# Kernel tuning notes

Measured on AMD Instinct MI355X. Metric: run time of the kernel, lower is better.

Reference implementation:

```python
import jax, jax.numpy as jnp
import numpy as np

NUM_NODES = 50000

def _gat_conv(x, edge_index, W, a_src, a_dst, b):
    # PyG GATConv, heads=1: h = x W ; e_ij = LeakyReLU(a_src.h_j + a_dst.h_i)
    # softmax over incoming edges of i ; out_i = sum_j alpha_ij h_j + b
    h = x @ W                                  # [N, F]
    src, dst = edge_index[0], edge_index[1]    # edge j->i : src=j, dst=i
    alpha_s = h @ a_src                        # [N]
    alpha_d = h @ a_dst                        # [N]
    e = jax.nn.leaky_relu(alpha_s[src] + alpha_d[dst], negative_slope=0.2)  # [E]
    # segment softmax over destination nodes
    e_max = jax.ops.segment_max(e, dst, num_segments=NUM_NODES)
    e_exp = jnp.exp(e - e_max[dst])
    denom = jax.ops.segment_sum(e_exp, dst, num_segments=NUM_NODES)
    coef = e_exp / denom[dst]                  # [E]
    out = jax.ops.segment_sum(h[src] * coef[:, None], dst, num_segments=NUM_NODES)
    return out + b

def setup_inputs() -> dict:
    key = jax.random.key(0)
    ks = jax.random.split(key, 10)
    N, E, IN, HID, OUT = NUM_NODES, 800000, 256, 256, 128
    x = jax.random.normal(ks[0], (N, IN), dtype=jnp.float32)
    edge_index = jax.random.randint(ks[1], (2, E), 0, N, dtype=jnp.int32)
    def glorot(k, shape):
        lim = float(np.sqrt(6.0 / (shape[0] + shape[-1])))
        return jax.random.uniform(k, shape, jnp.float32, -lim, lim)
    return {
        'x': x,
        'edge_index': edge_index,
        'W1': glorot(ks[2], (IN, HID)),
        'a_src1': glorot(ks[3], (HID,)),
        'a_dst1': glorot(ks[4], (HID,)),
        'b1': jnp.zeros((HID,), jnp.float32),
        'W2': glorot(ks[5], (HID, OUT)),
        'a_src2': glorot(ks[6], (OUT,)),
        'a_dst2': glorot(ks[7], (OUT,)),
        'b2': jnp.zeros((OUT,), jnp.float32),
    }

def reference(x, edge_index, W1, a_src1, a_dst1, b1, W2, a_src2, a_dst2, b2):
    # add self loops once (same edge_index used by both convs)
    ar = jnp.arange(NUM_NODES, dtype=edge_index.dtype)
    ei = jnp.concatenate([edge_index, jnp.stack([ar, ar])], axis=1)
    x1 = _gat_conv(x, ei, W1, a_src1, a_dst1, b1)
    h = jax.nn.relu(x1)          # dropout p=0.3 is identity in eval mode
    x2 = _gat_conv(h, ei, W2, a_src2, a_dst2, b2)
    return (x2, h)
```

## Files before the change

kernel.cpp:

```cpp
#include <hip/hip_runtime.h>
#include <hip/hip_bf16.h>

#define N_NODES 50000
#define E0      800000
#define ETOT    850000

typedef __bf16 bf16x8 __attribute__((ext_vector_type(8)));
typedef float  f32x4  __attribute__((ext_vector_type(4)));
typedef ushort u16x8  __attribute__((ext_vector_type(8)));
union B8 { u16x8 u; bf16x8 b; };

static __device__ __forceinline__ float b2f(ushort u) {
    union { uint u; float f; } x; x.u = ((uint)u) << 16; return x.f;
}
static __device__ __forceinline__ ushort f2bf(float f) {
    uint u = __builtin_bit_cast(uint, f);
    uint r = (u + 0x7FFFu + ((u >> 16) & 1u)) >> 16;
    return (ushort)r;
}

static __device__ __forceinline__ void gload16(const ushort* g, ushort* l) {
    __builtin_amdgcn_global_load_lds((const __attribute__((address_space(1))) unsigned int*)g,
                                     (__attribute__((address_space(3))) unsigned int*)l, 16, 0, 0);
}


__global__ __launch_bounds__(256) void k_deg(const int* __restrict__ ei, int* __restrict__ deg) {
    int e = blockIdx.x * 256 + threadIdx.x;
    if (e >= ETOT) return;
    int dst = (e < E0) ? ei[E0 + e] : (e - E0);
    atomicAdd(&deg[dst], 1);
}

__global__ __launch_bounds__(256) void k_scan1(const int* __restrict__ deg, int* __restrict__ offs,
                                               int* __restrict__ bsum) {
    __shared__ int buf[256];
    int tid = threadIdx.x;
    int i = blockIdx.x * 256 + tid;
    int v = (i < N_NODES) ? deg[i] : 0;
    buf[tid] = v;
    __syncthreads();
    for (int off = 1; off < 256; off <<= 1) {
        int t = (tid >= off) ? buf[tid - off] : 0;
        __syncthreads();
        buf[tid] += t;
        __syncthreads();
    }
    if (i < N_NODES) offs[i + 1] = buf[tid];
    if (tid == 255) bsum[blockIdx.x] = buf[255];
}

__global__ __launch_bounds__(256) void k_scan2(int* __restrict__ bsum, int nb) {
    __shared__ int buf[256];
    int tid = threadIdx.x;
    int v = (tid < nb) ? bsum[tid] : 0;
    buf[tid] = v;
    __syncthreads();
    for (int off = 1; off < 256; off <<= 1) {
        int t = (tid >= off) ? buf[tid - off] : 0;
        __syncthreads();
        buf[tid] += t;
        __syncthreads();
    }
    if (tid < nb) bsum[tid] = buf[tid] - v;
}

__global__ __launch_bounds__(256) void k_scan3(int* __restrict__ offs, const int* __restrict__ bsum,
                                               int* __restrict__ cursor) {
    int tid = threadIdx.x;
    int i = blockIdx.x * 256 + tid;
    if (i < N_NODES) {
        int v = offs[i + 1] + bsum[blockIdx.x];
        offs[i + 1] = v;
        cursor[i + 1] = v;
    }
    if (i == 0) { offs[0] = 0; cursor[0] = 0; }
}

__global__ __launch_bounds__(256) void k_scatter(const int* __restrict__ ei, int* __restrict__ cursor,
                                                 int* __restrict__ esrc) {
    int e = blockIdx.x * 256 + threadIdx.x;
    if (e >= ETOT) return;
    int src, dst;
    if (e < E0) { src = ei[e]; dst = ei[E0 + e]; }
    else        { src = e - E0; dst = src; }
    int pos = atomicAdd(&cursor[dst], 1);
    esrc[pos] = src;
}

__global__ __launch_bounds__(256) void k_splitT(const float* __restrict__ W, ushort* __restrict__ th,
                                                ushort* __restrict__ tl, int K, int N) {
    int i = blockIdx.x * 256 + threadIdx.x;
    if (i >= K * N) return;
    int n = i / K, k = i - n * K;
    float v = W[(size_t)k * N + n];
    ushort h = f2bf(v);
    th[(size_t)n * K + k] = h;
    tl[(size_t)n * K + k] = f2bf(v - b2f(h));
}

__global__ __launch_bounds__(256) void k_wvec(const float* __restrict__ W1, const float* __restrict__ s1v,
                                              const float* __restrict__ d1v, const float* __restrict__ W2,
                                              const float* __restrict__ s2v, const float* __restrict__ d2v,
                                              float* __restrict__ w1s, float* __restrict__ w1d,
                                              float* __restrict__ w2s, float* __restrict__ w2d) {
    int gw = (blockIdx.x * 256 + threadIdx.x) >> 6;
    int lane = threadIdx.x & 63;
    int vec = gw >> 8, kk = gw & 255;
    float a = 0.f;
    if (vec == 0)      { for (int n = lane; n < 256; n += 64) a += W1[(size_t)kk * 256 + n] * s1v[n]; }
    else if (vec == 1) { for (int n = lane; n < 256; n += 64) a += W1[(size_t)kk * 256 + n] * d1v[n]; }
    else if (vec == 2) { for (int n = lane; n < 128; n += 64) a += W2[(size_t)kk * 128 + n] * s2v[n]; }
    else               { for (int n = lane; n < 128; n += 64) a += W2[(size_t)kk * 128 + n] * d2v[n]; }
    for (int o = 32; o; o >>= 1) a += __shfl_down(a, o);
    if (lane == 0) {
        if (vec == 0) w1s[kk] = a;
        else if (vec == 1) w1d[kk] = a;
        else if (vec == 2) w2s[kk] = a;
        else w2d[kk] = a;
    }
}

__global__ __launch_bounds__(256) void k_prep1(const float* __restrict__ x, const float* __restrict__ w1s,
                                               const float* __restrict__ w1d, ushort* __restrict__ xb,
                                               float* __restrict__ as1, float* __restrict__ ad1) {
    int gw = (blockIdx.x * 256 + threadIdx.x) >> 6;
    int lane = threadIdx.x & 63;
    if (gw >= N_NODES) return;
    float4 v = *(const float4*)(x + (size_t)gw * 256 + lane * 4);
    ushort4 h;
    h.x = f2bf(v.x); h.y = f2bf(v.y); h.z = f2bf(v.z); h.w = f2bf(v.w);
    *(ushort4*)(xb + (size_t)gw * 256 + lane * 4) = h;
    float4 cs = *(const float4*)(w1s + lane * 4);
    float4 cd = *(const float4*)(w1d + lane * 4);
    float s = v.x * cs.x + v.y * cs.y + v.z * cs.z + v.w * cs.w;
    float d = v.x * cd.x + v.y * cd.y + v.z * cd.z + v.w * cd.w;
    for (int o = 32; o; o >>= 1) { s += __shfl_down(s, o); d += __shfl_down(d, o); }
    if (lane == 0) { as1[gw] = s; ad1[gw] = d; }
}


__global__ __launch_bounds__(256, 3) void k_gemm_mfma(const ushort* __restrict__ Ab,
                                                      const ushort* __restrict__ Bth,
                                                      const ushort* __restrict__ Btl,
                                                      ushort* __restrict__ Cb, int M, int Nn) {
    constexpr int K = 256;
    __shared__ ushort ldsA[2][128][32];
    __shared__ ushort ldsB[2][2][128][32];
    int tid = threadIdx.x;
    int wid = tid >> 6, lane = tid & 63;
    int wr = wid >> 1, wc = wid & 1;
    int bm = blockIdx.x * 128, bn = blockIdx.y * 128;
    int lr = lane & 15, lg = lane >> 4;

    int srow = tid >> 2, sk = (tid & 3) << 3;
    const ushort* ga0  = Ab  + (size_t)(bm + srow) * K + sk;
    const ushort* ga1  = Ab  + (size_t)(bm + srow + 64) * K + sk;
    const ushort* gbh0 = Bth + (size_t)(bn + srow) * K + sk;
    const ushort* gbh1 = Bth + (size_t)(bn + srow + 64) * K + sk;
    const ushort* gbl0 = Btl + (size_t)(bn + srow) * K + sk;
    const ushort* gbl1 = Btl + (size_t)(bn + srow + 64) * K + sk;

#define STAGE(B, KT) do {                                   \
    gload16(ga0  + (KT), &ldsA[B][srow][sk]);               \
    gload16(ga1  + (KT), &ldsA[B][srow + 64][sk]);          \
    gload16(gbh0 + (KT), &ldsB[B][0][srow][sk]);            \
    gload16(gbh1 + (KT), &ldsB[B][0][srow + 64][sk]);       \
    gload16(gbl0 + (KT), &ldsB[B][1][srow][sk]);            \
    gload16(gbl1 + (KT), &ldsB[B][1][srow + 64][sk]);       \
} while (0)

    f32x4 acc[4][4] = {};

    STAGE(0, 0);
    __syncthreads();

#pragma unroll
    for (int s = 0; s < 8; ++s) {
        const int buf = s & 1;
        if (s < 7) STAGE(buf ^ 1, (s + 1) * 32);
        bf16x8 ah[4], bh[4], bl[4];
#pragma unroll
        for (int m = 0; m < 4; ++m)
            ah[m] = *(const bf16x8*)&ldsA[buf][wr * 64 + m * 16 + lr][lg * 8];
#pragma unroll
        for (int n = 0; n < 4; ++n) {
            bh[n] = *(const bf16x8*)&ldsB[buf][0][wc * 64 + n * 16 + lr][lg * 8];
            bl[n] = *(const bf16x8*)&ldsB[buf][1][wc * 64 + n * 16 + lr][lg * 8];
        }
#pragma unroll
        for (int m = 0; m < 4; ++m)
#pragma unroll
            for (int n = 0; n < 4; ++n) {
                acc[m][n] = __builtin_amdgcn_mfma_f32_16x16x32_bf16(ah[m], bh[n], acc[m][n], 0, 0, 0);
                acc[m][n] = __builtin_amdgcn_mfma_f32_16x16x32_bf16(ah[m], bl[n], acc[m][n], 0, 0, 0);
            }
        __syncthreads();
    }
#undef STAGE
#pragma unroll
    for (int m = 0; m < 4; ++m)
#pragma unroll
        for (int r = 0; r < 4; ++r) {
            int row = bm + wr * 64 + m * 16 + lg * 4 + r;
            if (row < M) {
#pragma unroll
                for (int n = 0; n < 4; ++n) {
                    int col = bn + wc * 64 + n * 16 + lr;
                    Cb[(size_t)row * Nn + col] = f2bf(acc[m][n][r]);
                }
            }
        }
}

template <int F, bool RELU, bool WB, bool A2>
__global__ __launch_bounds__(256) void k_aggf(const int* __restrict__ offs, const int* __restrict__ esrc,
                                              const float* __restrict__ as, const float* __restrict__ ad,
                                              const ushort* __restrict__ H, const float* __restrict__ bias,
                                              float* __restrict__ out, ushort* __restrict__ hb,
                                              const float* __restrict__ w2s, const float* __restrict__ w2d,
                                              float* __restrict__ as2, float* __restrict__ ad2) {
    constexpr int V = F / 64;
    constexpr float THR = 8.f;
    int gw = (blockIdx.x * 256 + threadIdx.x) >> 6;
    int lane = threadIdx.x & 63;
    if (gw >= N_NODES) return;
    int s0 = offs[gw], s1 = offs[gw + 1];
    float adi = ad[gw];
    float m = -1e30f, ssum = 0.f;
    float acc[V] = {};
    int k = s0;
    for (; k + 7 < s1; k += 8) {
        int rr[8];
#pragma unroll
        for (int q = 0; q < 8; ++q) rr[q] = esrc[k + q];
        float ev[8];
#pragma unroll
        for (int q = 0; q < 8; ++q) ev[q] = as[rr[q]];
        float rows[8][V];
#pragma unroll
        for (int q = 0; q < 8; ++q) {
            if constexpr (V == 4) {
                ushort4 v = *(const ushort4*)(H + (size_t)rr[q] * F + lane * 4);
                rows[q][0] = b2f(v.x); rows[q][1] = b2f(v.y); rows[q][2] = b2f(v.z); rows[q][3] = b2f(v.w);
            } else {
                ushort2 v = *(const ushort2*)(H + (size_t)rr[q] * F + lane * 2);
                rows[q][0] = b2f(v.x); rows[q][1] = b2f(v.y);
            }
        }
        float em = -1e30f;
#pragma unroll
        for (int q = 0; q < 8; ++q) {
            float e = ev[q] + adi;
            e = e > 0.f ? e : 0.2f * e;
            ev[q] = e;
            em = fmaxf(em, e);
        }
        if (em > m + THR) {
            float sc = __expf(m - em);
            ssum *= sc;
#pragma unroll
            for (int j = 0; j < V; ++j) acc[j] *= sc;
            m = em;
        }
        float w[8];
#pragma unroll
        for (int q = 0; q < 8; ++q) w[q] = __expf(ev[q] - m);
#pragma unroll
        for (int q = 0; q < 8; ++q) ssum += w[q];
#pragma unroll
        for (int j = 0; j < V; ++j) {
            float a = acc[j];
#pragma unroll
            for (int q = 0; q < 8; ++q) a += w[q] * rows[q][j];
            acc[j] = a;
        }
    }
    for (; k + 3 < s1; k += 4) {
        int rr[4];
#pragma unroll
        for (int q = 0; q < 4; ++q) rr[q] = esrc[k + q];
        float ev[4];
#pragma unroll
        for (int q = 0; q < 4; ++q) ev[q] = as[rr[q]];
        float rows[4][V];
#pragma unroll
        for (int q = 0; q < 4; ++q) {
            if constexpr (V == 4) {
                ushort4 v = *(const ushort4*)(H + (size_t)rr[q] * F + lane * 4);
                rows[q][0] = b2f(v.x); rows[q][1] = b2f(v.y); rows[q][2] = b2f(v.z); rows[q][3] = b2f(v.w);
            } else {
                ushort2 v = *(const ushort2*)(H + (size_t)rr[q] * F + lane * 2);
                rows[q][0] = b2f(v.x); rows[q][1] = b2f(v.y);
            }
        }
        float em = -1e30f;
#pragma unroll
        for (int q = 0; q < 4; ++q) {
            float e = ev[q] + adi;
            e = e > 0.f ? e : 0.2f * e;
            ev[q] = e;
            em = fmaxf(em, e);
        }
        if (em > m + THR) {
            float sc = __expf(m - em);
            ssum *= sc;
#pragma unroll
            for (int j = 0; j < V; ++j) acc[j] *= sc;
            m = em;
        }
        float w[4];
#pragma unroll
        for (int q = 0; q < 4; ++q) w[q] = __expf(ev[q] - m);
#pragma unroll
        for (int q = 0; q < 4; ++q) ssum += w[q];
#pragma unroll
        for (int j = 0; j < V; ++j) {
            float a = acc[j];
#pragma unroll
            for (int q = 0; q < 4; ++q) a += w[q] * rows[q][j];
            acc[j] = a;
        }
    }
    for (; k < s1; ++k) {
        int r0 = esrc[k];
        float row0[V];
        if constexpr (V == 4) {
            ushort4 v0 = *(const ushort4*)(H + (size_t)r0 * F + lane * 4);
            row0[0] = b2f(v0.x); row0[1] = b2f(v0.y); row0[2] = b2f(v0.z); row0[3] = b2f(v0.w);
        } else {
            ushort2 v0 = *(const ushort2*)(H + (size_t)r0 * F + lane * 2);
            row0[0] = b2f(v0.x); row0[1] = b2f(v0.y);
        }
        float e0 = as[r0] + adi; e0 = e0 > 0.f ? e0 : 0.2f * e0;
        if (e0 > m + THR) {
            float sc = __expf(m - e0);
            ssum *= sc;
#pragma unroll
            for (int j = 0; j < V; ++j) acc[j] *= sc;
            m = e0;
        }
        float w0 = __expf(e0 - m);
        ssum += w0;
#pragma unroll
        for (int j = 0; j < V; ++j) acc[j] += w0 * row0[j];
    }
    float inv = 1.f / ssum;
    float r[V];
#pragma unroll
    for (int j = 0; j < V; ++j) {
        r[j] = acc[j] * inv + bias[lane * V + j];
        if (RELU) r[j] = fmaxf(r[j], 0.f);
    }
    if (V == 4) *(float4*)(out + (size_t)gw * F + lane * 4) = make_float4(r[0], r[1], r[2], r[3]);
    else        *(float2*)(out + (size_t)gw * F + lane * 2) = make_float2(r[0], r[1]);
    if constexpr (WB && V == 4) {
        ushort4 h4;
        h4.x = f2bf(r[0]); h4.y = f2bf(r[1]); h4.z = f2bf(r[2]); h4.w = f2bf(r[3]);
        *(ushort4*)(hb + (size_t)gw * F + lane * 4) = h4;
    }
    if constexpr (A2 && V == 4) {
        float4 cs = *(const float4*)(w2s + lane * 4);
        float4 cd = *(const float4*)(w2d + lane * 4);
        float s2 = r[0] * cs.x + r[1] * cs.y + r[2] * cs.z + r[3] * cs.w;
        float d2 = r[0] * cd.x + r[1] * cd.y + r[2] * cd.z + r[3] * cd.w;
        for (int o = 32; o; o >>= 1) { s2 += __shfl_down(s2, o); d2 += __shfl_down(d2, o); }
        if (lane == 0) { as2[gw] = s2; ad2[gw] = d2; }
    }
}


static inline size_t al256(size_t x) { return (x + 255) & ~(size_t)255; }

extern "C" void kernel_launch(void* const* d_in, const int* in_sizes, int n_in,
                              void* d_out, int out_size, void* d_ws, size_t ws_size,
                              hipStream_t stream) {
    const float* x   = (const float*)d_in[0];
    const int*   ei  = (const int*)d_in[1];
    const float* W1  = (const float*)d_in[2];
    const float* as1 = (const float*)d_in[3];
    const float* ad1 = (const float*)d_in[4];
    const float* b1  = (const float*)d_in[5];
    const float* W2  = (const float*)d_in[6];
    const float* as2 = (const float*)d_in[7];
    const float* ad2 = (const float*)d_in[8];
    const float* b2  = (const float*)d_in[9];

    float* out_x2 = (float*)d_out;
    float* out_h  = (float*)d_out + (size_t)N_NODES * 128;

    const size_t NM256 = (size_t)N_NODES * 256 * 2;
    const size_t PAD   = (size_t)128 * 256 * 2;
    char* base = (char*)d_ws;
    size_t off = 0;
    auto take = [&](size_t bytes) { char* p = base + off; off = al256(off + bytes); return p; };

    ushort* h1b  = (ushort*)take(NM256);
    ushort* xb   = (ushort*)take(NM256 + PAD);
    ushort* hb   = (ushort*)take(NM256 + PAD);
    ushort* w1th = (ushort*)take(256 * 256 * 2);
    ushort* w1tl = (ushort*)take(256 * 256 * 2);
    ushort* w2th = (ushort*)take(256 * 128 * 2);
    ushort* w2tl = (ushort*)take(256 * 128 * 2);
    float*  w1s  = (float*)take(256 * 4);
    float*  w1d  = (float*)take(256 * 4);
    float*  w2s  = (float*)take(256 * 4);
    float*  w2d  = (float*)take(256 * 4);
    float*  a1s  = (float*)take(N_NODES * 4);
    float*  a1d  = (float*)take(N_NODES * 4);
    float*  a2s  = (float*)take(N_NODES * 4);
    float*  a2d  = (float*)take(N_NODES * 4);
    int*    deg  = (int*)take(N_NODES * 4);
    int*    offs = (int*)take((N_NODES + 4) * 4);
    int*    curs = (int*)take((N_NODES + 4) * 4);
    int*    bsum = (int*)take(1024);
    int*    esrc = (int*)take((size_t)ETOT * 4);
    (void)ws_size;

    hipMemsetAsync(deg, 0, N_NODES * sizeof(int), stream);

    int nbE = (ETOT + 255) / 256;
    int nbN = (N_NODES + 255) / 256;
    int nbW = (N_NODES * 64 + 255) / 256;

    k_deg<<<nbE, 256, 0, stream>>>(ei, deg);
    k_scan1<<<nbN, 256, 0, stream>>>(deg, offs, bsum);
    k_scan2<<<1, 256, 0, stream>>>(bsum, nbN);
    k_scan3<<<nbN, 256, 0, stream>>>(offs, bsum, curs);
    k_scatter<<<nbE, 256, 0, stream>>>(ei, curs, esrc);

    k_splitT<<<(256 * 256 + 255) / 256, 256, 0, stream>>>(W1, w1th, w1tl, 256, 256);
    k_splitT<<<(256 * 128 + 255) / 256, 256, 0, stream>>>(W2, w2th, w2tl, 256, 128);
    k_wvec<<<256, 256, 0, stream>>>(W1, as1, ad1, W2, as2, ad2, w1s, w1d, w2s, w2d);
    k_prep1<<<nbW, 256, 0, stream>>>(x, w1s, w1d, xb, a1s, a1d);

    dim3 g1((N_NODES + 127) / 128, 2), g2((N_NODES + 127) / 128, 1);

    k_gemm_mfma<<<g1, 256, 0, stream>>>(xb, w1th, w1tl, h1b, N_NODES, 256);
    k_aggf<256, true, true, true><<<nbW, 256, 0, stream>>>(offs, esrc, a1s, a1d, h1b, b1,
                                                           out_h, hb, w2s, w2d, a2s, a2d);

    ushort* gb = h1b;
    k_gemm_mfma<<<g2, 256, 0, stream>>>(hb, w2th, w2tl, gb, N_NODES, 128);
    k_aggf<128, false, false, false><<<nbW, 256, 0, stream>>>(offs, esrc, a2s, a2d, gb, b2,
                                                              out_x2, nullptr, nullptr, nullptr,
                                                              nullptr, nullptr);
}
```

Before: 272.7 us.

## Split aggregation wave into two half-waves processing edges in parallel with wider loads

The GAT aggregation kernel now assigns each 32-lane half of a wave to alternate edges. Each lane loads 8 or 4 bf16 features per row instead of 4 or 2, and the half-wave partial sums and running max are merged with xor shuffles. This is meant to raise per-lane load width and the number of rows in flight for the gather-bound softmax aggregation, at the cost of extra shuffles and more registers. Separately, the W transpose/split and attention-vector kernels are fused into one launch to cut launch overhead.

```diff
diff --git a/kernel.cpp b/kernel.cpp
--- a/kernel.cpp
+++ b/kernel.cpp
@@ -8,6 +8,7 @@
 typedef __bf16 bf16x8 __attribute__((ext_vector_type(8)));
 typedef float  f32x4  __attribute__((ext_vector_type(4)));
 typedef ushort u16x8  __attribute__((ext_vector_type(8)));
+typedef ushort u16x4  __attribute__((ext_vector_type(4)));
 union B8 { u16x8 u; bf16x8 b; };
 
 static __device__ __forceinline__ float b2f(ushort u) {
@@ -88,36 +89,44 @@
     esrc[pos] = src;
 }
 
-__global__ __launch_bounds__(256) void k_splitT(const float* __restrict__ W, ushort* __restrict__ th,
-                                                ushort* __restrict__ tl, int K, int N) {
-    int i = blockIdx.x * 256 + threadIdx.x;
-    if (i >= K * N) return;
-    int n = i / K, k = i - n * K;
-    float v = W[(size_t)k * N + n];
-    ushort h = f2bf(v);
-    th[(size_t)n * K + k] = h;
-    tl[(size_t)n * K + k] = f2bf(v - b2f(h));
-}
-
-__global__ __launch_bounds__(256) void k_wvec(const float* __restrict__ W1, const float* __restrict__ s1v,
-                                              const float* __restrict__ d1v, const float* __restrict__ W2,
-                                              const float* __restrict__ s2v, const float* __restrict__ d2v,
-                                              float* __restrict__ w1s, float* __restrict__ w1d,
-                                              float* __restrict__ w2s, float* __restrict__ w2d) {
-    int gw = (blockIdx.x * 256 + threadIdx.x) >> 6;
-    int lane = threadIdx.x & 63;
-    int vec = gw >> 8, kk = gw & 255;
-    float a = 0.f;
-    if (vec == 0)      { for (int n = lane; n < 256; n += 64) a += W1[(size_t)kk * 256 + n] * s1v[n]; }
-    else if (vec == 1) { for (int n = lane; n < 256; n += 64) a += W1[(size_t)kk * 256 + n] * d1v[n]; }
-    else if (vec == 2) { for (int n = lane; n < 128; n += 64) a += W2[(size_t)kk * 128 + n] * s2v[n]; }
-    else               { for (int n = lane; n < 128; n += 64) a += W2[(size_t)kk * 128 + n] * d2v[n]; }
-    for (int o = 32; o; o >>= 1) a += __shfl_down(a, o);
-    if (lane == 0) {
-        if (vec == 0) w1s[kk] = a;
-        else if (vec == 1) w1d[kk] = a;
-        else if (vec == 2) w2s[kk] = a;
-        else w2d[kk] = a;
+__global__ __launch_bounds__(256) void k_wprep(const float* __restrict__ W1, const float* __restrict__ W2,
+                                               const float* __restrict__ s1v, const float* __restrict__ d1v,
+                                               const float* __restrict__ s2v, const float* __restrict__ d2v,
+                                               ushort* __restrict__ w1th, ushort* __restrict__ w1tl,
+                                               ushort* __restrict__ w2th, ushort* __restrict__ w2tl,
+                                               float* __restrict__ w1s, float* __restrict__ w1d,
+                                               float* __restrict__ w2s, float* __restrict__ w2d) {
+    int b = blockIdx.x, t = threadIdx.x;
+    if (b < 256) {
+        int i = b * 256 + t;
+        int n = i >> 8, k = i & 255;
+        float v = W1[(size_t)k * 256 + n];
+        ushort h = f2bf(v);
+        w1th[(size_t)n * 256 + k] = h;
+        w1tl[(size_t)n * 256 + k] = f2bf(v - b2f(h));
+    } else if (b < 384) {
+        int i = (b - 256) * 256 + t;
+        int n = i >> 8, k = i & 255;
+        float v = W2[(size_t)k * 128 + n];
+        ushort h = f2bf(v);
+        w2th[(size_t)n * 256 + k] = h;
+        w2tl[(size_t)n * 256 + k] = f2bf(v - b2f(h));
+    } else {
+        int gw = ((b - 384) * 256 + t) >> 6;
+        int lane = t & 63;
+        int vec = gw >> 8, kk = gw & 255;
+        float a = 0.f;
+        if (vec == 0)      { for (int n = lane; n < 256; n += 64) a += W1[(size_t)kk * 256 + n] * s1v[n]; }
+        else if (vec == 1) { for (int n = lane; n < 256; n += 64) a += W1[(size_t)kk * 256 + n] * d1v[n]; }
+        else if (vec == 2) { for (int n = lane; n < 128; n += 64) a += W2[(size_t)kk * 128 + n] * s2v[n]; }
+        else               { for (int n = lane; n < 128; n += 64) a += W2[(size_t)kk * 128 + n] * d2v[n]; }
+        for (int o = 32; o; o >>= 1) a += __shfl_down(a, o);
+        if (lane == 0) {
+            if (vec == 0) w1s[kk] = a;
+            else if (vec == 1) w1d[kk] = a;
+            else if (vec == 2) w2s[kk] = a;
+            else w2d[kk] = a;
+        }
     }
 }
 
@@ -220,80 +229,29 @@
                                               float* __restrict__ out, ushort* __restrict__ hb,
                                               const float* __restrict__ w2s, const float* __restrict__ w2d,
                                               float* __restrict__ as2, float* __restrict__ ad2) {
-    constexpr int V = F / 64;
+    constexpr int FL = F / 32;
     constexpr float THR = 8.f;
+    using Vec = typename std::conditional<FL == 8, u16x8, u16x4>::type;
     int gw = (blockIdx.x * 256 + threadIdx.x) >> 6;
     int lane = threadIdx.x & 63;
+    int sub = lane >> 5, sl = lane & 31;
     if (gw >= N_NODES) return;
     int s0 = offs[gw], s1 = offs[gw + 1];
     float adi = ad[gw];
     float m = -1e30f, ssum = 0.f;
-    float acc[V] = {};
+    float acc[FL] = {};
+    const ushort* Hp = H + sl * FL;
     int k = s0;
     for (; k + 7 < s1; k += 8) {
-        int rr[8];
-#pragma unroll
-        for (int q = 0; q < 8; ++q) rr[q] = esrc[k + q];
-        float ev[8];
-#pragma unroll
-        for (int q = 0; q < 8; ++q) ev[q] = as[rr[q]];
-        float rows[8][V];
-#pragma unroll
-        for (int q = 0; q < 8; ++q) {
-            if constexpr (V == 4) {
-                ushort4 v = *(const ushort4*)(H + (size_t)rr[q] * F + lane * 4);
-                rows[q][0] = b2f(v.x); rows[q][1] = b2f(v.y); rows[q][2] = b2f(v.z); rows[q][3] = b2f(v.w);
-            } else {
-                ushort2 v = *(const ushort2*)(H + (size_t)rr[q] * F + lane * 2);
-                rows[q][0] = b2f(v.x); rows[q][1] = b2f(v.y);
-            }
-        }
-        float em = -1e30f;
-#pragma unroll
-        for (int q = 0; q < 8; ++q) {
-            float e = ev[q] + adi;
-            e = e > 0.f ? e : 0.2f * e;
-            ev[q] = e;
-            em = fmaxf(em, e);
-        }
-        if (em > m + THR) {
-            float sc = __expf(m - em);
-            ssum *= sc;
-#pragma unroll
-            for (int j = 0; j < V; ++j) acc[j] *= sc;
-            m = em;
-        }
-        float w[8];
-#pragma unroll
-        for (int q = 0; q < 8; ++q) w[q] = __expf(ev[q] - m);
-#pragma unroll
-        for (int q = 0; q < 8; ++q) ssum += w[q];
-#pragma unroll
-        for (int j = 0; j < V; ++j) {
-            float a = acc[j];
-#pragma unroll
-            for (int q = 0; q < 8; ++q) a += w[q] * rows[q][j];
-            acc[j] = a;
-        }
-    }
-    for (; k + 3 < s1; k += 4) {
         int rr[4];
 #pragma unroll
-        for (int q = 0; q < 4; ++q) rr[q] = esrc[k + q];
+        for (int q = 0; q < 4; ++q) rr[q] = esrc[k + 2 * q + sub];
         float ev[4];
 #pragma unroll
         for (int q = 0; q < 4; ++q) ev[q] = as[rr[q]];
-        float rows[4][V];
-#pragma unroll
-        for (int q = 0; q < 4; ++q) {
-            if constexpr (V == 4) {
-                ushort4 v = *(const ushort4*)(H + (size_t)rr[q] * F + lane * 4);
-                rows[q][0] = b2f(v.x); rows[q][1] = b2f(v.y); rows[q][2] = b2f(v.z); rows[q][3] = b2f(v.w);
-            } else {
-                ushort2 v = *(const ushort2*)(H + (size_t)rr[q] * F + lane * 2);
-                rows[q][0] = b2f(v.x); rows[q][1] = b2f(v.y);
-            }
-        }
+        Vec rows[4];
+#pragma unroll
+        for (int q = 0; q < 4; ++q) rows[q] = *(const Vec*)(Hp + (size_t)rr[q] * F);
         float em = -1e30f;
 #pragma unroll
         for (int q = 0; q < 4; ++q) {
@@ -302,11 +260,12 @@
             ev[q] = e;
             em = fmaxf(em, e);
         }
+        em = fmaxf(em, __shfl_xor(em, 32));
         if (em > m + THR) {
             float sc = __expf(m - em);
             ssum *= sc;
 #pragma unroll
-            for (int j = 0; j < V; ++j) acc[j] *= sc;
+            for (int j = 0; j < FL; ++j) acc[j] *= sc;
             m = em;
         }
         float w[4];
@@ -315,56 +274,67 @@
 #pragma unroll
         for (int q = 0; q < 4; ++q) ssum += w[q];
 #pragma unroll
-        for (int j = 0; j < V; ++j) {
+        for (int j = 0; j < FL; ++j) {
             float a = acc[j];
 #pragma unroll
-            for (int q = 0; q < 4; ++q) a += w[q] * rows[q][j];
+            for (int q = 0; q < 4; ++q) a += w[q] * b2f(rows[q][j]);
             acc[j] = a;
         }
     }
-    for (; k < s1; ++k) {
-        int r0 = esrc[k];
-        float row0[V];
-        if constexpr (V == 4) {
-            ushort4 v0 = *(const ushort4*)(H + (size_t)r0 * F + lane * 4);
-            row0[0] = b2f(v0.x); row0[1] = b2f(v0.y); row0[2] = b2f(v0.z); row0[3] = b2f(v0.w);
+    for (; k < s1; k += 2) {
+        int idx = k + sub;
+        bool val = idx < s1;
+        int r0 = esrc[val ? idx : s1 - 1];
+        Vec v = *(const Vec*)(Hp + (size_t)r0 * F);
+        float e = as[r0] + adi;
+        e = e > 0.f ? e : 0.2f * e;
+        if (!val) e = -3e30f;
+        float em = fmaxf(e, __shfl_xor(e, 32));
+        if (em > m + THR) {
+            float sc = __expf(m - em);
+            ssum *= sc;
+#pragma unroll
+            for (int j = 0; j < FL; ++j) acc[j] *= sc;
+            m = em;
+        }
+        float w0 = val ? __expf(e - m) : 0.f;
+        ssum += w0;
+#pragma unroll
+        for (int j = 0; j < FL; ++j) acc[j] += w0 * b2f(v[j]);
+    }
+#pragma unroll
+    for (int j = 0; j < FL; ++j) acc[j] += __shfl_xor(acc[j], 32);
+    ssum += __shfl_xor(ssum, 32);
+
+    float inv = 1.f / ssum;
+    float r[FL];
+#pragma unroll
+    for (int j = 0; j < FL; ++j) {
+        r[j] = acc[j] * inv + bias[sl * FL + j];
+        if (RELU) r[j] = fmaxf(r[j], 0.f);
+    }
+    if (sub == 0) {
+        if constexpr (FL == 8) {
+            *(float4*)(out + (size_t)gw * F + sl * 8)     = make_float4(r[0], r[1], r[2], r[3]);
+            *(float4*)(out + (size_t)gw * F + sl * 8 + 4) = make_float4(r[4], r[5], r[6], r[7]);
         } else {
-            ushort2 v0 = *(const ushort2*)(H + (size_t)r0 * F + lane * 2);
-            row0[0] = b2f(v0.x); row0[1] = b2f(v0.y);
-        }
-        float e0 = as[r0] + adi; e0 = e0 > 0.f ? e0 : 0.2f * e0;
-        if (e0 > m + THR) {
-            float sc = __expf(m - e0);
-            ssum *= sc;
-#pragma unroll
-            for (int j = 0; j < V; ++j) acc[j] *= sc;
-            m = e0;
-        }
-        float w0 = __expf(e0 - m);
-        ssum += w0;
-#pragma unroll
-        for (int j = 0; j < V; ++j) acc[j] += w0 * row0[j];
-    }
-    float inv = 1.f / ssum;
-    float r[V];
-#pragma unroll
-    for (int j = 0; j < V; ++j) {
-        r[j] = acc[j] * inv + bias[lane * V + j];
-        if (RELU) r[j] = fmaxf(r[j], 0.f);
-    }
-    if (V == 4) *(float4*)(out + (size_t)gw * F + lane * 4) = make_float4(r[0], r[1], r[2], r[3]);
-    else        *(float2*)(out + (size_t)gw * F + lane * 2) = make_float2(r[0], r[1]);
-    if constexpr (WB && V == 4) {
-        ushort4 h4;
-        h4.x = f2bf(r[0]); h4.y = f2bf(r[1]); h4.z = f2bf(r[2]); h4.w = f2bf(r[3]);
-        *(ushort4*)(hb + (size_t)gw * F + lane * 4) = h4;
-    }
-    if constexpr (A2 && V == 4) {
-        float4 cs = *(const float4*)(w2s + lane * 4);
-        float4 cd = *(const float4*)(w2d + lane * 4);
-        float s2 = r[0] * cs.x + r[1] * cs.y + r[2] * cs.z + r[3] * cs.w;
-        float d2 = r[0] * cd.x + r[1] * cd.y + r[2] * cd.z + r[3] * cd.w;
-        for (int o = 32; o; o >>= 1) { s2 += __shfl_down(s2, o); d2 += __shfl_down(d2, o); }
+            *(float4*)(out + (size_t)gw * F + sl * 4) = make_float4(r[0], r[1], r[2], r[3]);
+        }
+        if constexpr (WB && FL == 8) {
+            u16x8 hv;
+#pragma unroll
+            for (int j = 0; j < 8; ++j) hv[j] = f2bf(r[j]);
+            *(u16x8*)(hb + (size_t)gw * F + sl * 8) = hv;
+        }
+    }
+    if constexpr (A2 && FL == 8) {
+        float s2 = 0.f, d2 = 0.f;
+#pragma unroll
+        for (int j = 0; j < 8; ++j) {
+            s2 += r[j] * w2s[sl * 8 + j];
+            d2 += r[j] * w2d[sl * 8 + j];
+        }
+        for (int o = 16; o; o >>= 1) { s2 += __shfl_down(s2, o, 32); d2 += __shfl_down(d2, o, 32); }
         if (lane == 0) { as2[gw] = s2; ad2[gw] = d2; }
     }
 }
@@ -400,8 +370,8 @@
     ushort* hb   = (ushort*)take(NM256 + PAD);
     ushort* w1th = (ushort*)take(256 * 256 * 2);
     ushort* w1tl = (ushort*)take(256 * 256 * 2);
-    ushort* w2th = (ushort*)take(256 * 128 * 2);
-    ushort* w2tl = (ushort*)take(256 * 128 * 2);
+    ushort* w2th = (ushort*)take(256 * 256 * 2);
+    ushort* w2tl = (ushort*)take(256 * 256 * 2);
     float*  w1s  = (float*)take(256 * 4);
     float*  w1d  = (float*)take(256 * 4);
     float*  w2s  = (float*)take(256 * 4);
@@ -429,9 +399,8 @@
     k_scan3<<<nbN, 256, 0, stream>>>(offs, bsum, curs);
     k_scatter<<<nbE, 256, 0, stream>>>(ei, curs, esrc);
 
-    k_splitT<<<(256 * 256 + 255) / 256, 256, 0, stream>>>(W1, w1th, w1tl, 256, 256);
-    k_splitT<<<(256 * 128 + 255) / 256, 256, 0, stream>>>(W2, w2th, w2tl, 256, 128);
-    k_wvec<<<256, 256, 0, stream>>>(W1, as1, ad1, W2, as2, ad2, w1s, w1d, w2s, w2d);
+    k_wprep<<<640, 256, 0, stream>>>(W1, W2, as1, ad1, as2, ad2,
+                                     w1th, w1tl, w2th, w2tl, w1s, w1d, w2s, w2d);
     k_prep1<<<nbW, 256, 0, stream>>>(x, w1s, w1d, xb, a1s, a1d);
 
     dim3 g1((N_NODES + 127) / 128, 2), g2((N_NODES + 127) / 128, 1);
```

New measurement: 267.8 us. Within noise of the previous version (-1.8%).
